# Performance work log

Measured on AMD Instinct MI355X. Metric: run time of the kernel, lower is better.

The kernel has to match this reference:

```python
import jax, jax.numpy as jnp
import numpy as np

B, N, DIM, H = 2, 2048, 1024, 16
D = DIM // H  # head_dim = 64


def setup_inputs() -> dict:
    key = jax.random.key(0)
    ks = jax.random.split(key, 3)
    w_scale = 0.02
    return {
        "x": jax.random.normal(ks[0], (B, N, DIM), dtype=jnp.float32),
        "Wqkv": jax.random.normal(ks[1], (DIM, 3 * DIM), dtype=jnp.float32) * w_scale,
        "bqkv": jnp.zeros((3 * DIM,), dtype=jnp.float32),
        "Wproj": jax.random.normal(ks[2], (DIM, DIM), dtype=jnp.float32) * w_scale,
        "bproj": jnp.zeros((DIM,), dtype=jnp.float32),
        "sigma": jnp.ones((1,), dtype=jnp.float32),
        "gamma": jnp.ones((1,), dtype=jnp.float32),
    }


def reference(x, Wqkv, bqkv, Wproj, bproj, sigma, gamma):
    b, n, c = x.shape
    # qkv projection -> (B, N, 3, H, D)
    qkv = (x @ Wqkv + bqkv).reshape(b, n, 3, H, D)
    q = jnp.transpose(qkv[:, :, 0], (0, 2, 1, 3))  # [B, H, N, D]
    k = jnp.transpose(qkv[:, :, 1], (0, 2, 1, 3))
    v = jnp.transpose(qkv[:, :, 2], (0, 2, 1, 3))
    scale = 1.0 / jnp.sqrt(jnp.asarray(D, dtype=x.dtype))
    scores = jnp.einsum("bhqd,bhkd->bhqk", q, k) * scale  # [B, H, N, N]
    # divisive normalization (cortical gain control) over key axis
    denom = sigma + jnp.sqrt(jnp.mean(scores * scores, axis=-1, keepdims=True))
    scores = gamma * scores / denom
    attn = jax.nn.softmax(scores, axis=-1)
    out = jnp.einsum("bhqk,bhkd->bhqd", attn, v)  # [B, H, N, D]
    out = jnp.transpose(out, (0, 2, 1, 3)).reshape(b, n, c)
    return out @ Wproj + bproj
```

## Files before the change

kernel.cpp:

```cpp
#include <hip/hip_runtime.h>

typedef __attribute__((ext_vector_type(4))) float f32x4;
typedef __attribute__((ext_vector_type(8))) _Float16 f16x8;
typedef __attribute__((ext_vector_type(4))) _Float16 f16x4;
typedef __attribute__((ext_vector_type(2))) _Float16 f16x2;

#define MFMA_F16(a, b, c) __builtin_amdgcn_mfma_f32_16x16x32_f16(a, b, c, 0, 0, 0)

__device__ __forceinline__ void gload_lds16(const void* g, void* l) {
  __builtin_amdgcn_global_load_lds(
      (const __attribute__((address_space(1))) void*)g,
      (__attribute__((address_space(3))) void*)l, 16, 0, 0);
}
__device__ __forceinline__ f16x2 pk2(float a, float b) {
  return __builtin_bit_cast(f16x2, __builtin_amdgcn_cvt_pkrtz(a, b));
}
__device__ __forceinline__ void pipe_barrier_v4() {
  asm volatile("s_waitcnt vmcnt(4) lgkmcnt(0)" ::: "memory");
  __builtin_amdgcn_sched_barrier(0);
  __builtin_amdgcn_s_barrier();
}
__device__ __forceinline__ void pipe_barrier_v3() {
  asm volatile("s_waitcnt vmcnt(3) lgkmcnt(0)" ::: "memory");
  __builtin_amdgcn_sched_barrier(0);
  __builtin_amdgcn_s_barrier();
}
__device__ __forceinline__ void pipe_barrier_v2() {
  asm volatile("s_waitcnt vmcnt(2) lgkmcnt(0)" ::: "memory");
  __builtin_amdgcn_sched_barrier(0);
  __builtin_amdgcn_s_barrier();
}
__device__ __forceinline__ void pipe_barrier_v0() {
  asm volatile("s_waitcnt vmcnt(0) lgkmcnt(0)" ::: "memory");
  __builtin_amdgcn_sched_barrier(0);
  __builtin_amdgcn_s_barrier();
}

__global__ __launch_bounds__(256) void prep_kernel(
    const float* __restrict__ x, _Float16* __restrict__ xf,
    const float* __restrict__ Wqkv, _Float16* __restrict__ wqt,
    const float* __restrict__ Wproj, _Float16* __restrict__ wpt) {
  __shared__ float tile[32][33];
  const int bx = blockIdx.x;
  if (bx < 4096) {
    const int i = bx * 256 + threadIdx.x;
    f32x4 v = *(const f32x4*)(x + (size_t)i * 4);
    f16x4 h;
#pragma unroll
    for (int j = 0; j < 4; ++j) h[j] = (_Float16)v[j];
    *(f16x4*)(xf + (size_t)i * 4) = h;
    return;
  }
  const float* W;
  _Float16* wt;
  int N, n0, k0;
  if (bx < 7168) {
    const int t = bx - 4096;
    W = Wqkv; wt = wqt; N = 3072;
    n0 = (t % 96) * 32; k0 = (t / 96) * 32;
  } else {
    const int t = bx - 7168;
    W = Wproj; wt = wpt; N = 1024;
    n0 = (t % 32) * 32; k0 = (t / 32) * 32;
  }
  const int tx = threadIdx.x & 31, ty = threadIdx.x >> 5;
#pragma unroll
  for (int j = 0; j < 32; j += 8)
    tile[ty + j][tx] = W[(size_t)(k0 + ty + j) * N + n0 + tx];
  __syncthreads();
#pragma unroll
  for (int j = 0; j < 32; j += 8)
    wt[(size_t)(n0 + ty + j) * 1024 + k0 + tx] = (_Float16)tile[tx][ty + j];
}

__global__ __launch_bounds__(256) void gemm_qkv_kernel(
    const _Float16* __restrict__ xf, const _Float16* __restrict__ wt,
    const float* __restrict__ bias, _Float16* __restrict__ QF,
    _Float16* __restrict__ KF, _Float16* __restrict__ KT,
    _Float16* __restrict__ VT) {
  __shared__ __attribute__((aligned(16))) _Float16 lg[24576];
  const int tid = threadIdx.x, lane = tid & 63, w = tid >> 6;
  const int wg = blockIdx.x;
  const int cx = wg & 7, c = wg >> 3;
  const int bxl = (cx & 1) * 12 + c % 12;
  const int byl = (cx >> 1) * 8 + c / 12;
  const int m0 = byl * 128, n0 = bxl * 128;
  const int wr = (w >> 1) * 64, wc = (w & 1) * 64;
  f32x4 acc[4][4] = {};

  const int srow = lane >> 2;
  const int scol = (((lane & 3) ^ ((lane >> 3) & 3)) * 8);
  const int fr = lane & 15, fg = lane >> 4;
  const int rswz = (fr >> 1) & 3;

  auto stageT = [&](int buf, int k0) {
#pragma unroll
    for (int j = 0; j < 2; ++j) {
      const int rbase = 32 * w + 16 * j;
      const int r = rbase + srow;
      gload_lds16(xf + (size_t)(m0 + r) * 1024 + k0 + scol,
                  &lg[buf * 8192 + rbase * 32]);
      gload_lds16(wt + (size_t)(n0 + r) * 1024 + k0 + scol,
                  &lg[buf * 8192 + 4096 + rbase * 32]);
    }
  };
  auto mfma_step = [&](int ab) {
    f16x8 af[4], bfr[4];
#pragma unroll
    for (int m = 0; m < 4; ++m)
      af[m] = *(const f16x8*)&lg[ab + (wr + 16 * m + fr) * 32 + ((fg ^ rswz) * 8)];
#pragma unroll
    for (int n = 0; n < 4; ++n)
      bfr[n] = *(const f16x8*)&lg[ab + 4096 + (wc + 16 * n + fr) * 32 + ((fg ^ rswz) * 8)];
#pragma unroll
    for (int m = 0; m < 4; ++m)
#pragma unroll
      for (int n = 0; n < 4; ++n) acc[m][n] = MFMA_F16(af[m], bfr[n], acc[m][n]);
  };

  stageT(0, 0);
  stageT(1, 32);
  pipe_barrier_v4();
  for (int T = 0; T < 30; T += 3) {
#pragma unroll
    for (int s = 0; s < 3; ++s) {
      stageT((s + 2) % 3, (T + s + 2) * 32);
      mfma_step(s * 8192);
      pipe_barrier_v4();
    }
  }
  mfma_step(0);
  pipe_barrier_v0();
  mfma_step(8192);
  pipe_barrier_v0();

  const int fq = fg * 4;
#pragma unroll
  for (int n = 0; n < 4; ++n) {
    const float bv = bias[n0 + wc + 16 * n + fr];
#pragma unroll
    for (int m = 0; m < 4; ++m)
#pragma unroll
      for (int i = 0; i < 4; ++i)
        lg[(wr + 16 * m + fq + i) * 129 + wc + 16 * n + fr] =
            (_Float16)(acc[m][n][i] + bv);
  }
  __syncthreads();
  const int b = m0 >> 11, nnb = m0 & 2047;
  const int h0 = 2 * (bxl & 7);
  const int sPhase = bxl >> 3;
  if (sPhase <= 1) {
    _Float16* __restrict__ dst = (sPhase == 0) ? QF : KF;
#pragma unroll
    for (int p = 0; p < 8; ++p) {
      const int r = p * 16 + (tid >> 4);
      const int cc = tid & 15;
      f16x8 vals;
#pragma unroll
      for (int j = 0; j < 8; ++j) vals[j] = lg[r * 129 + cc * 8 + j];
      const int h = cc >> 3, d = (cc & 7) * 8;
      *(f16x8*)&dst[((size_t)((b * 16 + h0 + h) * 2048 + nnb + r)) * 64 + d] = vals;
    }
  }
  if (sPhase >= 1) {
    _Float16* __restrict__ T = (sPhase == 1) ? KT : VT;
#pragma unroll
    for (int p = 0; p < 8; ++p) {
      const int lr = p * 16 + (tid >> 4);
      const int cc = tid & 15;
      f16x8 vals;
#pragma unroll
      for (int j = 0; j < 8; ++j) vals[j] = lg[(cc * 8 + j) * 129 + lr];
      const int h = lr >> 6, d = lr & 63;
      *(f16x8*)&T[((size_t)((b * 16 + h0 + h) * 64 + d)) * 2048 + nnb + cc * 8] = vals;
    }
  }
}

__global__ __launch_bounds__(256) void gram_partial_kernel(
    const _Float16* __restrict__ KT, float* __restrict__ GP) {
  __shared__ __attribute__((aligned(16))) _Float16 sT[3][4096];
  const int tid = threadIdx.x, lane = tid & 63, w = tid >> 6;
  const int bh = blockIdx.x >> 2, qt = blockIdx.x & 3;
  const _Float16* src = KT + (size_t)bh * 64 * 2048 + qt * 512;
  const int s_r = lane >> 3, s_cg = lane & 7;
  const int fr = lane & 15, fg = lane >> 4;
  const int kswz = fr & 7;

  auto stage = [&](int buf, int n0) {
#pragma unroll
    for (int j = 0; j < 2; ++j) {
      const int rbase = 8 * w + 32 * j;
      gload_lds16(src + (size_t)(rbase + s_r) * 2048 + n0 + ((s_cg ^ s_r) * 8),
                  &sT[buf][rbase * 64]);
    }
  };

  f32x4 acc[4] = {};
  stage(0, 0);
  stage(1, 64);
  pipe_barrier_v2();
  int cur = 0;
#pragma unroll
  for (int t = 0; t < 8; ++t) {
    if (t < 6) {
      const int nb = (cur + 2 >= 3) ? cur - 1 : cur + 2;
      stage(nb, (t + 2) * 64);
    }
    f16x8 af[2];
#pragma unroll
    for (int ks = 0; ks < 2; ++ks)
      af[ks] = *(const f16x8*)&sT[cur][(16 * w + fr) * 64 + (((ks * 4 + fg) ^ kswz) * 8)];
#pragma unroll
    for (int nt = 0; nt < 4; ++nt)
#pragma unroll
      for (int ks = 0; ks < 2; ++ks)
        acc[nt] = MFMA_F16(
            af[ks],
            *(const f16x8*)&sT[cur][(16 * nt + fr) * 64 + (((ks * 4 + fg) ^ kswz) * 8)],
            acc[nt]);
    if (t < 6) pipe_barrier_v2(); else pipe_barrier_v0();
    cur = (cur + 1 == 3) ? 0 : cur + 1;
  }
  float* dst = GP + (size_t)blockIdx.x * 4096;
#pragma unroll
  for (int nt = 0; nt < 4; ++nt)
#pragma unroll
    for (int i = 0; i < 4; ++i)
      dst[(16 * w + fg * 4 + i) * 64 + 16 * nt + fr] = acc[nt][i];
}

__global__ __launch_bounds__(256) void gram_reduce_kernel(
    const float* __restrict__ GP, _Float16* __restrict__ GH,
    _Float16* __restrict__ GL) {
  const int bh = blockIdx.x >> 2, seg = blockIdx.x & 3;
  const int e0 = seg * 1024 + threadIdx.x * 4;
  const float* p = GP + (size_t)bh * 4 * 4096 + e0;
  f32x4 s = *(const f32x4*)p;
  s += *(const f32x4*)(p + 4096);
  s += *(const f32x4*)(p + 8192);
  s += *(const f32x4*)(p + 12288);
  f16x4 gh, gl;
#pragma unroll
  for (int j = 0; j < 4; ++j) {
    gh[j] = (_Float16)s[j];
    gl[j] = (_Float16)(s[j] - (float)gh[j]);
  }
  *(f16x4*)&GH[(size_t)bh * 4096 + e0] = gh;
  *(f16x4*)&GL[(size_t)bh * 4096 + e0] = gl;
}

__global__ __launch_bounds__(256) void attn_kernel(
    const _Float16* __restrict__ QF, const _Float16* __restrict__ KF,
    const _Float16* __restrict__ VT, const _Float16* __restrict__ GH,
    const _Float16* __restrict__ GL, _Float16* __restrict__ OB,
    const float* __restrict__ sigma_p, const float* __restrict__ gamma_p) {
  __shared__ __attribute__((aligned(16))) _Float16 lds[32768];

  const int tid = threadIdx.x, lane = tid & 63, w = tid >> 6;
  const int wg = blockIdx.x;
  const int c = wg >> 3;
  const int bh = (wg & 7) * 4 + (c >> 4);
  const int q0 = (c & 15) * 128;
  const size_t base = (size_t)bh * (2048 * 64);
  const float sigma = sigma_p[0], gamma = gamma_p[0];
  const int fr = lane & 15, fg = lane >> 4;
  const int s_r = lane >> 3, s_cg = lane & 7;
  const int kswz = fr & 7;

  const _Float16* Kbh = KF + base;
  const _Float16* Tbh = VT + base;

  f16x8 qf[2][2];
#pragma unroll
  for (int m = 0; m < 2; ++m)
#pragma unroll
    for (int ks = 0; ks < 2; ++ks)
      qf[m][ks] = *(const f16x8*)(QF + base +
                                  (size_t)(q0 + 32 * w + 16 * m + fr) * 64 +
                                  ks * 32 + fg * 8);

  auto stage64 = [&](int dstoff, const _Float16* g, int srcstride) {
#pragma unroll
    for (int j = 0; j < 2; ++j) {
      const int rbase = 8 * w + 32 * j;
      gload_lds16(g + (size_t)(rbase + s_r) * srcstride + ((s_cg ^ s_r) * 8),
                  &lds[dstoff + rbase * 64]);
    }
  };
  auto stage64K = [&](int dstoff, const _Float16* g) {
#pragma unroll
    for (int j = 0; j < 2; ++j) {
      const int rbase = 8 * w + 32 * j;
      const int r = rbase + s_r;
      const int pr = (r & 0x23) | ((r & 0x0C) << 1) | ((r & 0x10) >> 2);
      gload_lds16(g + (size_t)pr * 64 + ((s_cg ^ s_r) * 8),
                  &lds[dstoff + rbase * 64]);
    }
  };
  auto stage_tile = [&](int b, int kb) {
    stage64K(b * 4096, Kbh + (size_t)kb * 4096);
    stage64(16384 + b * 4096, Tbh + kb * 64, 2048);
  };

  stage64(0, GH + (size_t)bh * 4096, 64);
  stage64(4096, GL + (size_t)bh * 4096, 64);
  __syncthreads();
  float minvl2[2];
  float* Yp = (float*)&lds[8192 + w * 2048];
#pragma unroll
  for (int m = 0; m < 2; ++m) {
    f32x4 yacc[4] = {};
#pragma unroll
    for (int nt = 0; nt < 4; ++nt) {
#pragma unroll
      for (int ks = 0; ks < 2; ++ks) {
        const int off = (16 * nt + fr) * 64 + (((ks * 4 + fg) ^ kswz) * 8);
        yacc[nt] = MFMA_F16(qf[m][ks], *(const f16x8*)&lds[off], yacc[nt]);
        yacc[nt] = MFMA_F16(qf[m][ks], *(const f16x8*)&lds[4096 + off], yacc[nt]);
      }
    }
#pragma unroll
    for (int nt = 0; nt < 4; ++nt)
#pragma unroll
      for (int i = 0; i < 4; ++i) Yp[(fg * 4 + i) * 64 + 16 * nt + fr] = yacc[nt][i];
    float zp = 0.0f;
#pragma unroll
    for (int ks = 0; ks < 2; ++ks) {
      const f32x4 y0 = *(const f32x4*)&Yp[fr * 64 + ks * 32 + fg * 8];
      const f32x4 y1 = *(const f32x4*)&Yp[fr * 64 + ks * 32 + fg * 8 + 4];
#pragma unroll
      for (int cc = 0; cc < 4; ++cc) {
        zp += y0[cc] * (float)qf[m][ks][cc];
        zp += y1[cc] * (float)qf[m][ks][cc + 4];
      }
    }
    zp += __shfl_xor(zp, 16);
    zp += __shfl_xor(zp, 32);
    const float rms = sqrtf(fmaxf(zp, 0.0f)) * (1.0f / 362.038672f);
    minvl2[m] = gamma / (sigma + rms) * 0.125f * 1.44269504f;
  }
  __syncthreads();

  float lsum[2] = {};
  f32x4 oacc[2][4] = {};

  auto qk_tile = [&](int kbuf, f32x4 (&pn)[2][4]) {
#pragma unroll
    for (int n = 0; n < 4; ++n) {
      const int offb = kbuf * 4096 + (16 * n + fr) * 64;
      const f16x8 kf0 = *(const f16x8*)&lds[offb + ((fg ^ kswz) * 8)];
      const f16x8 kf1 = *(const f16x8*)&lds[offb + (((4 + fg) ^ kswz) * 8)];
#pragma unroll
      for (int m = 0; m < 2; ++m) {
        f32x4 a = {};
        a = MFMA_F16(kf0, qf[m][0], a);
        a = MFMA_F16(kf1, qf[m][1], a);
        pn[m][n] = a;
      }
    }
  };
  auto exp_pack = [&](f32x4 (&pn)[2][4], f16x8 (&pa)[2][2]) {
#pragma unroll
    for (int m = 0; m < 2; ++m) {
#pragma unroll
      for (int n = 0; n < 4; ++n)
#pragma unroll
        for (int i = 0; i < 4; ++i) {
          const float p = __builtin_amdgcn_exp2f(pn[m][n][i] * minvl2[m]);
          lsum[m] += p;
          pn[m][n][i] = p;
        }
#pragma unroll
      for (int k2 = 0; k2 < 2; ++k2) {
        const f16x2 c0 = pk2(pn[m][2 * k2][0], pn[m][2 * k2][1]);
        const f16x2 c1 = pk2(pn[m][2 * k2][2], pn[m][2 * k2][3]);
        const f16x2 c2 = pk2(pn[m][2 * k2 + 1][0], pn[m][2 * k2 + 1][1]);
        const f16x2 c3 = pk2(pn[m][2 * k2 + 1][2], pn[m][2 * k2 + 1][3]);
        pa[m][k2][0] = c0[0]; pa[m][k2][1] = c0[1];
        pa[m][k2][2] = c1[0]; pa[m][k2][3] = c1[1];
        pa[m][k2][4] = c2[0]; pa[m][k2][5] = c2[1];
        pa[m][k2][6] = c3[0]; pa[m][k2][7] = c3[1];
      }
    }
  };
  auto pv_tile = [&](int vbuf, f16x8 (&pa)[2][2]) {
#pragma unroll
    for (int k2 = 0; k2 < 2; ++k2) {
#pragma unroll
      for (int nf = 0; nf < 4; ++nf) {
        const int off = 16384 + vbuf * 4096 + (16 * nf + fr) * 64 +
                        (((k2 * 4 + fg) ^ kswz) * 8);
        const f16x8 vt = *(const f16x8*)&lds[off];
        oacc[0][nf] = MFMA_F16(vt, pa[0][k2], oacc[0][nf]);
        oacc[1][nf] = MFMA_F16(vt, pa[1][k2], oacc[1][nf]);
      }
    }
  };

  f32x4 pn[2][4];
  f16x8 pa[2][2][2];

  stage_tile(0, 0);
  stage_tile(1, 1);
  stage_tile(2, 2);
  pipe_barrier_v4();
  qk_tile(0, pn);
  exp_pack(pn, pa[0]);

  for (int T = 0; T < 28; T += 4) {
#pragma unroll
    for (int s = 0; s < 4; ++s) {
      stage_tile((s + 3) & 3, T + s + 3);
      __builtin_amdgcn_s_setprio(1);
      qk_tile((s + 1) & 3, pn);
      __builtin_amdgcn_s_setprio(0);
      __builtin_amdgcn_s_setprio(1);
      pv_tile(s & 3, pa[s & 1]);
      __builtin_amdgcn_s_setprio(0);
      exp_pack(pn, pa[(s + 1) & 1]);
      pipe_barrier_v4();
    }
  }
  {
    stage_tile(3, 31);
    __builtin_amdgcn_s_setprio(1); qk_tile(1, pn); __builtin_amdgcn_s_setprio(0);
    __builtin_amdgcn_s_setprio(1); pv_tile(0, pa[0]); __builtin_amdgcn_s_setprio(0);
    exp_pack(pn, pa[1]);
    pipe_barrier_v4();
    __builtin_amdgcn_s_setprio(1); qk_tile(2, pn); __builtin_amdgcn_s_setprio(0);
    __builtin_amdgcn_s_setprio(1); pv_tile(1, pa[1]); __builtin_amdgcn_s_setprio(0);
    exp_pack(pn, pa[0]);
    pipe_barrier_v0();
    __builtin_amdgcn_s_setprio(1); qk_tile(3, pn); __builtin_amdgcn_s_setprio(0);
    __builtin_amdgcn_s_setprio(1); pv_tile(2, pa[0]); __builtin_amdgcn_s_setprio(0);
    exp_pack(pn, pa[1]);
    pipe_barrier_v0();
    __builtin_amdgcn_s_setprio(1); pv_tile(3, pa[1]); __builtin_amdgcn_s_setprio(0);
  }

  float inv[2];
#pragma unroll
  for (int m = 0; m < 2; ++m) {
    lsum[m] += __shfl_xor(lsum[m], 16);
    lsum[m] += __shfl_xor(lsum[m], 32);
    inv[m] = 1.0f / lsum[m];
  }

  const int b = bh >> 4, h = bh & 15;
#pragma unroll
  for (int m = 0; m < 2; ++m) {
    const size_t orow = (size_t)(b * 2048 + q0 + 32 * w + 16 * m + fr);
#pragma unroll
    for (int nf = 0; nf < 4; ++nf) {
      f16x4 ov;
#pragma unroll
      for (int i = 0; i < 4; ++i) ov[i] = (_Float16)(oacc[m][nf][i] * inv[m]);
      *(f16x4*)&OB[orow * 1024 + h * 64 + 16 * nf + 4 * fg] = ov;
    }
  }
}

__global__ __launch_bounds__(256) void gemm_proj_kernel(
    const _Float16* __restrict__ A, const _Float16* __restrict__ Bt,
    const float* __restrict__ bias, float* __restrict__ out) {
  __shared__ __attribute__((aligned(16))) _Float16 lg[18432];
  const int tid = threadIdx.x, lane = tid & 63, w = tid >> 6;
  const int wg = blockIdx.x;
  const int c = wg >> 3;
  const int bxl = c & 7;
  const int byl = (wg & 7) * 8 + (c >> 3);
  const int m0 = byl * 64, n0 = bxl * 128;
  const int wr = (w >> 1) * 32, wc = (w & 1) * 64;
  f32x4 acc[2][4] = {};
  const int srow = lane >> 2;
  const int scol = (((lane & 3) ^ ((lane >> 3) & 3)) * 8);
  const int fr = lane & 15, fg = lane >> 4;
  const int rswz = (fr >> 1) & 3;

  auto stageT = [&](int buf, int k0) {
    {
      const int rbase = 16 * w;
      gload_lds16(A + (size_t)(m0 + rbase + srow) * 1024 + k0 + scol,
                  &lg[buf * 6144 + rbase * 32]);
    }
#pragma unroll
    for (int j = 0; j < 2; ++j) {
      const int rbase = 32 * w + 16 * j;
      gload_lds16(Bt + (size_t)(n0 + rbase + srow) * 1024 + k0 + scol,
                  &lg[buf * 6144 + 2048 + rbase * 32]);
    }
  };
  auto mfma_step = [&](int ab) {
    f16x8 af[2], bfr[4];
#pragma unroll
    for (int m = 0; m < 2; ++m)
      af[m] = *(const f16x8*)&lg[ab + (wr + 16 * m + fr) * 32 + ((fg ^ rswz) * 8)];
#pragma unroll
    for (int n = 0; n < 4; ++n)
      bfr[n] = *(const f16x8*)&lg[ab + 2048 + (wc + 16 * n + fr) * 32 + ((fg ^ rswz) * 8)];
#pragma unroll
    for (int m = 0; m < 2; ++m)
#pragma unroll
      for (int n = 0; n < 4; ++n) acc[m][n] = MFMA_F16(af[m], bfr[n], acc[m][n]);
  };

  stageT(0, 0);
  stageT(1, 32);
  pipe_barrier_v3();
  for (int T = 0; T < 30; T += 3) {
#pragma unroll
    for (int s = 0; s < 3; ++s) {
      stageT((s + 2) % 3, (T + s + 2) * 32);
      mfma_step(s * 6144);
      pipe_barrier_v3();
    }
  }
  mfma_step(0);
  pipe_barrier_v0();
  mfma_step(6144);
  pipe_barrier_v0();

  const int fq = fg * 4;
#pragma unroll
  for (int n = 0; n < 4; ++n) {
    const int col = n0 + wc + 16 * n + fr;
    const float bv = bias[col];
#pragma unroll
    for (int m = 0; m < 2; ++m) {
#pragma unroll
      for (int i = 0; i < 4; ++i) {
        const int row = m0 + wr + 16 * m + fq + i;
        out[(size_t)row * 1024 + col] = acc[m][n][i] + bv;
      }
    }
  }
}

extern "C" void kernel_launch(void* const* d_in, const int* in_sizes, int n_in,
                              void* d_out, int out_size, void* d_ws, size_t ws_size,
                              hipStream_t stream) {
  const float* x = (const float*)d_in[0];
  const float* Wqkv = (const float*)d_in[1];
  const float* bqkv = (const float*)d_in[2];
  const float* Wproj = (const float*)d_in[3];
  const float* bproj = (const float*)d_in[4];
  const float* sigma = (const float*)d_in[5];
  const float* gamma = (const float*)d_in[6];
  float* out = (float*)d_out;

  char* ws = (char*)d_ws;
  const size_t MB = 1024 * 1024;
  _Float16* XF  = (_Float16*)(ws + 0 * MB);
  _Float16* WQT = (_Float16*)(ws + 8 * MB);
  _Float16* WPT = (_Float16*)(ws + 14 * MB);
  _Float16* QF  = (_Float16*)(ws + 16 * MB);
  _Float16* KF  = (_Float16*)(ws + 24 * MB);
  _Float16* VT  = (_Float16*)(ws + 32 * MB);
  _Float16* KT  = (_Float16*)(ws + 40 * MB);
  _Float16* OB  = (_Float16*)(ws + 40 * MB);
  _Float16* GH  = (_Float16*)(ws + 8 * MB);
  _Float16* GL  = (_Float16*)(ws + 8 * MB + 512 * 1024);
  float*    GP  = (float*)(ws + 9 * MB);

  prep_kernel<<<8192, 256, 0, stream>>>(x, XF, Wqkv, WQT, Wproj, WPT);
  gemm_qkv_kernel<<<768, 256, 0, stream>>>(XF, WQT, bqkv, QF, KF, KT, VT);
  gram_partial_kernel<<<128, 256, 0, stream>>>(KT, GP);
  gram_reduce_kernel<<<128, 256, 0, stream>>>(GP, GH, GL);
  attn_kernel<<<512, 256, 0, stream>>>(QF, KF, VT, GH, GL, OB, sigma, gamma);
  gemm_proj_kernel<<<512, 256, 0, stream>>>(OB, WPT, bproj, out);
}
```

Measured before the change: 120.6 us.

## Split attention over key halves with combine kernel and MFMA row sums

```diff
diff --git a/kernel.cpp b/kernel.cpp
--- a/kernel.cpp
+++ b/kernel.cpp
@@ -253,15 +253,19 @@
 __global__ __launch_bounds__(256) void attn_kernel(
     const _Float16* __restrict__ QF, const _Float16* __restrict__ KF,
     const _Float16* __restrict__ VT, const _Float16* __restrict__ GH,
-    const _Float16* __restrict__ GL, _Float16* __restrict__ OB,
+    const _Float16* __restrict__ GL, _Float16* __restrict__ PO0,
+    _Float16* __restrict__ PO1, float* __restrict__ LS,
     const float* __restrict__ sigma_p, const float* __restrict__ gamma_p) {
-  __shared__ __attribute__((aligned(16))) _Float16 lds[32768];
+  __shared__ __attribute__((aligned(16))) _Float16 lds[24576];
 
   const int tid = threadIdx.x, lane = tid & 63, w = tid >> 6;
   const int wg = blockIdx.x;
   const int c = wg >> 3;
-  const int bh = (wg & 7) * 4 + (c >> 4);
-  const int q0 = (c & 15) * 128;
+  const int bh = (wg & 7) * 4 + (c >> 5);
+  const int rem = c & 31;
+  const int q0 = (rem >> 1) * 128;
+  const int kh = rem & 1;
+  const int kt0 = kh * 16;
   const size_t base = (size_t)bh * (2048 * 64);
   const float sigma = sigma_p[0], gamma = gamma_p[0];
   const int fr = lane & 15, fg = lane >> 4;
@@ -300,7 +304,7 @@
   };
   auto stage_tile = [&](int b, int kb) {
     stage64K(b * 4096, Kbh + (size_t)kb * 4096);
-    stage64(16384 + b * 4096, Tbh + kb * 64, 2048);
+    stage64(12288 + b * 4096, Tbh + kb * 64, 2048);
   };
 
   stage64(0, GH + (size_t)bh * 4096, 64);
@@ -340,12 +344,32 @@
     const float rms = sqrtf(fmaxf(zp, 0.0f)) * (1.0f / 362.038672f);
     minvl2[m] = gamma / (sigma + rms) * 0.125f * 1.44269504f;
   }
+#pragma unroll
+  for (int m = 0; m < 2; ++m)
+#pragma unroll
+    for (int ks = 0; ks < 2; ++ks) {
+      f16x8 q = qf[m][ks], r;
+#pragma unroll
+      for (int j = 0; j < 4; ++j) {
+        const f16x2 t = pk2((float)q[2 * j] * minvl2[m],
+                            (float)q[2 * j + 1] * minvl2[m]);
+        r[2 * j] = t[0];
+        r[2 * j + 1] = t[1];
+      }
+      qf[m][ks] = r;
+    }
   __syncthreads();
 
-  float lsum[2] = {};
   f32x4 oacc[2][4] = {};
-
-  auto qk_tile = [&](int kbuf, f32x4 (&pn)[2][4]) {
+  f32x4 lacc[2] = {};
+  f16x8 ones;
+#pragma unroll
+  for (int j = 0; j < 8; ++j) ones[j] = (_Float16)1.0f;
+
+  f32x4 pn[2][4];
+  f16x8 pa[2][2];
+
+  auto qk_tile = [&](int kbuf) {
 #pragma unroll
     for (int n = 0; n < 4; ++n) {
       const int offb = kbuf * 4096 + (16 * n + fr) * 64;
@@ -360,17 +384,14 @@
       }
     }
   };
-  auto exp_pack = [&](f32x4 (&pn)[2][4], f16x8 (&pa)[2][2]) {
+  auto exp_pack = [&]() {
 #pragma unroll
     for (int m = 0; m < 2; ++m) {
 #pragma unroll
       for (int n = 0; n < 4; ++n)
 #pragma unroll
-        for (int i = 0; i < 4; ++i) {
-          const float p = __builtin_amdgcn_exp2f(pn[m][n][i] * minvl2[m]);
-          lsum[m] += p;
-          pn[m][n][i] = p;
-        }
+        for (int i = 0; i < 4; ++i)
+          pn[m][n][i] = __builtin_amdgcn_exp2f(pn[m][n][i]);
 #pragma unroll
       for (int k2 = 0; k2 < 2; ++k2) {
         const f16x2 c0 = pk2(pn[m][2 * k2][0], pn[m][2 * k2][1]);
@@ -384,81 +405,82 @@
       }
     }
   };
-  auto pv_tile = [&](int vbuf, f16x8 (&pa)[2][2]) {
+  auto pv_tile = [&](int vbuf) {
 #pragma unroll
     for (int k2 = 0; k2 < 2; ++k2) {
 #pragma unroll
       for (int nf = 0; nf < 4; ++nf) {
-        const int off = 16384 + vbuf * 4096 + (16 * nf + fr) * 64 +
+        const int off = 12288 + vbuf * 4096 + (16 * nf + fr) * 64 +
                         (((k2 * 4 + fg) ^ kswz) * 8);
         const f16x8 vt = *(const f16x8*)&lds[off];
         oacc[0][nf] = MFMA_F16(vt, pa[0][k2], oacc[0][nf]);
         oacc[1][nf] = MFMA_F16(vt, pa[1][k2], oacc[1][nf]);
       }
-    }
-  };
-
-  f32x4 pn[2][4];
-  f16x8 pa[2][2][2];
-
-  stage_tile(0, 0);
-  stage_tile(1, 1);
-  stage_tile(2, 2);
+      lacc[0] = MFMA_F16(ones, pa[0][k2], lacc[0]);
+      lacc[1] = MFMA_F16(ones, pa[1][k2], lacc[1]);
+    }
+  };
+  auto iter = [&](int s) {
+    __builtin_amdgcn_s_setprio(1);
+    qk_tile(s);
+    __builtin_amdgcn_s_setprio(0);
+    exp_pack();
+    __builtin_amdgcn_s_setprio(1);
+    pv_tile(s);
+    __builtin_amdgcn_s_setprio(0);
+  };
+
+  stage_tile(0, kt0 + 0);
+  stage_tile(1, kt0 + 1);
   pipe_barrier_v4();
-  qk_tile(0, pn);
-  exp_pack(pn, pa[0]);
-
-  for (int T = 0; T < 28; T += 4) {
-#pragma unroll
-    for (int s = 0; s < 4; ++s) {
-      stage_tile((s + 3) & 3, T + s + 3);
-      __builtin_amdgcn_s_setprio(1);
-      qk_tile((s + 1) & 3, pn);
-      __builtin_amdgcn_s_setprio(0);
-      __builtin_amdgcn_s_setprio(1);
-      pv_tile(s & 3, pa[s & 1]);
-      __builtin_amdgcn_s_setprio(0);
-      exp_pack(pn, pa[(s + 1) & 1]);
+  for (int T = 0; T < 12; T += 3) {
+#pragma unroll
+    for (int s = 0; s < 3; ++s) {
+      stage_tile((s + 2) % 3, kt0 + T + s + 2);
+      iter(s);
       pipe_barrier_v4();
     }
   }
-  {
-    stage_tile(3, 31);
-    __builtin_amdgcn_s_setprio(1); qk_tile(1, pn); __builtin_amdgcn_s_setprio(0);
-    __builtin_amdgcn_s_setprio(1); pv_tile(0, pa[0]); __builtin_amdgcn_s_setprio(0);
-    exp_pack(pn, pa[1]);
-    pipe_barrier_v4();
-    __builtin_amdgcn_s_setprio(1); qk_tile(2, pn); __builtin_amdgcn_s_setprio(0);
-    __builtin_amdgcn_s_setprio(1); pv_tile(1, pa[1]); __builtin_amdgcn_s_setprio(0);
-    exp_pack(pn, pa[0]);
-    pipe_barrier_v0();
-    __builtin_amdgcn_s_setprio(1); qk_tile(3, pn); __builtin_amdgcn_s_setprio(0);
-    __builtin_amdgcn_s_setprio(1); pv_tile(2, pa[0]); __builtin_amdgcn_s_setprio(0);
-    exp_pack(pn, pa[1]);
-    pipe_barrier_v0();
-    __builtin_amdgcn_s_setprio(1); pv_tile(3, pa[1]); __builtin_amdgcn_s_setprio(0);
-  }
-
-  float inv[2];
+  stage_tile(2, kt0 + 14); iter(0); pipe_barrier_v4();
+  stage_tile(0, kt0 + 15); iter(1); pipe_barrier_v4();
+  iter(2); pipe_barrier_v0();
+  iter(0);
+
+  _Float16* __restrict__ PO = (kh == 0) ? PO0 : PO1;
+  const int b = bh >> 4, h = bh & 15;
 #pragma unroll
   for (int m = 0; m < 2; ++m) {
-    lsum[m] += __shfl_xor(lsum[m], 16);
-    lsum[m] += __shfl_xor(lsum[m], 32);
-    inv[m] = 1.0f / lsum[m];
-  }
-
-  const int b = bh >> 4, h = bh & 15;
-#pragma unroll
-  for (int m = 0; m < 2; ++m) {
-    const size_t orow = (size_t)(b * 2048 + q0 + 32 * w + 16 * m + fr);
+    const int q = q0 + 32 * w + 16 * m + fr;
+    if (fg == 0) LS[(size_t)(kh * 32 + bh) * 2048 + q] = lacc[m][0];
+    const size_t orow = (size_t)(b * 2048 + q);
 #pragma unroll
     for (int nf = 0; nf < 4; ++nf) {
       f16x4 ov;
 #pragma unroll
-      for (int i = 0; i < 4; ++i) ov[i] = (_Float16)(oacc[m][nf][i] * inv[m]);
-      *(f16x4*)&OB[orow * 1024 + h * 64 + 16 * nf + 4 * fg] = ov;
-    }
-  }
+      for (int i = 0; i < 4; ++i) ov[i] = (_Float16)(oacc[m][nf][i]);
+      *(f16x4*)&PO[orow * 1024 + h * 64 + 16 * nf + 4 * fg] = ov;
+    }
+  }
+}
+
+__global__ __launch_bounds__(256) void combine_kernel(
+    const _Float16* __restrict__ PO0, const _Float16* __restrict__ PO1,
+    const float* __restrict__ LS, _Float16* __restrict__ OB) {
+  const int g = blockIdx.x * 256 + threadIdx.x;
+  const size_t e = (size_t)g * 8;
+  const int orow = (int)(e >> 10), col = (int)(e & 1023);
+  const int h = col >> 6;
+  const int b = orow >> 11, nn = orow & 2047;
+  const size_t li = (size_t)(b * 16 + h) * 2048 + nn;
+  const float ls = LS[li] + LS[li + 32 * 2048];
+  const float inv = 1.0f / ls;
+  const f16x8 a = *(const f16x8*)&PO0[e];
+  const f16x8 bb = *(const f16x8*)&PO1[e];
+  f16x8 o;
+#pragma unroll
+  for (int j = 0; j < 8; ++j)
+    o[j] = (_Float16)(((float)a[j] + (float)bb[j]) * inv);
+  *(f16x8*)&OB[e] = o;
 }
 
 __global__ __launch_bounds__(256) void gemm_proj_kernel(
@@ -558,15 +580,19 @@
   _Float16* KF  = (_Float16*)(ws + 24 * MB);
   _Float16* VT  = (_Float16*)(ws + 32 * MB);
   _Float16* KT  = (_Float16*)(ws + 40 * MB);
-  _Float16* OB  = (_Float16*)(ws + 40 * MB);
   _Float16* GH  = (_Float16*)(ws + 8 * MB);
   _Float16* GL  = (_Float16*)(ws + 8 * MB + 512 * 1024);
   float*    GP  = (float*)(ws + 9 * MB);
+  float*    LS  = (float*)(ws + 11 * MB);
+  _Float16* PO0 = (_Float16*)(ws + 0 * MB);
+  _Float16* PO1 = (_Float16*)(ws + 40 * MB);
+  _Float16* OB  = (_Float16*)(ws + 40 * MB);
 
   prep_kernel<<<8192, 256, 0, stream>>>(x, XF, Wqkv, WQT, Wproj, WPT);
   gemm_qkv_kernel<<<768, 256, 0, stream>>>(XF, WQT, bqkv, QF, KF, KT, VT);
   gram_partial_kernel<<<128, 256, 0, stream>>>(KT, GP);
   gram_reduce_kernel<<<128, 256, 0, stream>>>(GP, GH, GL);
-  attn_kernel<<<512, 256, 0, stream>>>(QF, KF, VT, GH, GL, OB, sigma, gamma);
+  attn_kernel<<<1024, 256, 0, stream>>>(QF, KF, VT, GH, GL, PO0, PO1, LS, sigma, gamma);
+  combine_kernel<<<2048, 256, 0, stream>>>(PO0, PO1, LS, OB);
   gemm_proj_kernel<<<512, 256, 0, stream>>>(OB, WPT, bproj, out);
 }
```

New measurement: 126.3 us. +4.7%, slower.
